# Performance work log

Measured on AMD Instinct MI355X. Metric: run time of the kernel, lower is better.

## Reference

```python
import jax, jax.numpy as jnp
import numpy as np

NPOINT = 2048
RADIUS = 0.4
NSAMPLE = 32
BN_EPS = 1e-5


def setup_inputs() -> dict:
    key = jax.random.key(0)
    ks = jax.random.split(key, 6)
    B, N, C = 8, 8192, 64
    xyz = jax.random.normal(ks[0], (B, N, 3), jnp.float32)
    points = jax.random.normal(ks[1], (B, N, C), jnp.float32)
    W1 = jax.random.normal(ks[2], (3 + C, 64), jnp.float32) * 0.1
    W2 = jax.random.normal(ks[3], (64, 64), jnp.float32) * 0.1
    W3 = jax.random.normal(ks[4], (64, 128), jnp.float32) * 0.1
    return dict(
        xyz=xyz, points=points,
        W1=W1, g1=jnp.ones(64), b1=jnp.zeros(64),
        W2=W2, g2=jnp.ones(64), b2=jnp.zeros(64),
        W3=W3, g3=jnp.ones(128), b3=jnp.zeros(128),
    )


def _furthest_point_sample(xyz, npoint):
    # xyz: (B, N, 3) -> (B, npoint) int32. Sequential max-min scan, batched.
    B, N, _ = xyz.shape

    def step(carry, _):
        dists, last = carry
        p = jnp.take_along_axis(xyz, last[:, None, None], axis=1)  # (B,1,3)
        d2 = jnp.sum((xyz - p) ** 2, axis=-1)                       # (B,N)
        dists = jnp.minimum(dists, d2)
        nxt = jnp.argmax(dists, axis=-1).astype(jnp.int32)
        return (dists, nxt), nxt

    init = (jnp.full((B, N), 1e10, xyz.dtype), jnp.zeros((B,), jnp.int32))
    _, idx = jax.lax.scan(step, init, None, length=npoint - 1)      # (npoint-1, B)
    idx = jnp.concatenate([jnp.zeros((1, B), jnp.int32), idx], axis=0)
    return idx.T                                                    # (B, npoint)


def _ball_query(xyz, new_xyz, radius, nsample):
    # For each centroid take the first nsample point indices (in original order)
    # within `radius`; pad with the first found index (CUDA ball_query semantics).
    B, N, _ = xyz.shape
    d2 = jnp.sum((new_xyz[:, :, None, :] - xyz[:, None, :, :]) ** 2, axis=-1)  # (B,S,N)
    mask = d2 < radius * radius
    key = jnp.where(mask, jnp.arange(N, dtype=jnp.int32), N)
    srt = jnp.sort(key, axis=-1)[..., :nsample]                     # (B,S,K)
    first = srt[..., :1]
    first = jnp.where(first == N, 0, first)                         # empty ball -> index 0
    return jnp.where(srt == N, first, srt)


def _gather(pts, idx):
    # pts: (B,N,D), idx: (B,...) -> (B,...,D)
    return jax.vmap(lambda p, i: p[i])(pts, idx)


def reference(xyz, points, W1, g1, b1, W2, g2, b2, W3, g3, b3):
    fps_idx = _furthest_point_sample(xyz, NPOINT)                   # (B,S)
    new_xyz = _gather(xyz, fps_idx)                                 # (B,S,3)
    idx = _ball_query(xyz, new_xyz, RADIUS, NSAMPLE)                # (B,S,K)
    grouped_xyz = _gather(xyz, idx) - new_xyz[:, :, None, :]        # (B,S,K,3)
    grouped_pts = _gather(points, idx)                              # (B,S,K,C)
    feats = jnp.concatenate([grouped_xyz, grouped_pts], axis=-1)    # (B,S,K,3+C)
    for W, g, b in ((W1, g1, b1), (W2, g2, b2), (W3, g3, b3)):
        feats = feats @ W                                           # 1x1 conv
        m = feats.mean(axis=(0, 1, 2))
        v = feats.var(axis=(0, 1, 2))                               # biased, torch BN train mode
        feats = g * (feats - m) * jax.lax.rsqrt(v + BN_EPS) + b
        feats = jax.nn.relu(feats)
    new_points = feats.max(axis=2)                                  # max over nsample -> (B,S,mlp[-1])
    return new_xyz, new_points
```

## Files before the change

kernel.cpp:

```cpp
#include <hip/hip_runtime.h>

constexpr int B_ = 8, N_ = 8192, NPOINT_ = 2048, NSAMPLE_ = 32;
constexpr int M_ROWS = B_ * NPOINT_ * NSAMPLE_;
constexpr int NGROUP = B_ * NPOINT_;
constexpr size_t OFF_NXF   = 0;
constexpr size_t OFF_IDX   = 196608;
constexpr size_t OFF_WF    = 1245184;
constexpr size_t OFF_GB    = 1311488;
constexpr size_t OFF_STATS = 1313536;
constexpr size_t OFF_NP    = 1315584;
constexpr size_t OFF_FLAG  = 1317632;
constexpr size_t OFF_MAXB  = 2097152;

__device__ __forceinline__ float bf2f(unsigned short u) {
  union { unsigned u; float f; } x; x.u = ((unsigned)u) << 16; return x.f;
}
__device__ __forceinline__ float lo16f(unsigned u) {
  union { unsigned u; float f; } x; x.u = u << 16; return x.f;
}
__device__ __forceinline__ float hi16f(unsigned u) {
  union { unsigned u; float f; } x; x.u = u & 0xffff0000u; return x.f;
}
__device__ __forceinline__ unsigned short f2bf(float f) {
  union { float f; unsigned u; } x; x.f = f;
  unsigned u = x.u + 0x7FFFu + ((x.u >> 16) & 1u);
  return (unsigned short)(u >> 16);
}
__device__ __forceinline__ void unpack8(uint4 u, float* x) {
  x[0] = bf2f((unsigned short)(u.x & 0xffffu)); x[1] = bf2f((unsigned short)(u.x >> 16));
  x[2] = bf2f((unsigned short)(u.y & 0xffffu)); x[3] = bf2f((unsigned short)(u.y >> 16));
  x[4] = bf2f((unsigned short)(u.z & 0xffffu)); x[5] = bf2f((unsigned short)(u.z >> 16));
  x[6] = bf2f((unsigned short)(u.w & 0xffffu)); x[7] = bf2f((unsigned short)(u.w >> 16));
}
__device__ __forceinline__ float ldf(const void* p, size_t i, bool bf) {
  return bf ? bf2f(((const unsigned short*)p)[i]) : ((const float*)p)[i];
}
__device__ __forceinline__ void stf(void* p, size_t i, bool bf, float v) {
  if (bf) ((unsigned short*)p)[i] = f2bf(v);
  else    ((float*)p)[i] = v;
}

extern "C" __global__ void detect_kernel(const unsigned short* __restrict__ xyz,
                                         int* __restrict__ flag) {
  if (threadIdx.x == 0 && blockIdx.x == 0) {
    int sane = 0;
    for (int k = 0; k < 32; ++k) {
      int e = (xyz[2 * k] >> 7) & 0xff;
      if (e >= 90 && e <= 140) ++sane;
    }
    *flag = (sane >= 24) ? 1 : 0;
  }
}

extern "C" __global__ void prep_kernel(
    const void* W1, const void* W2, const void* W3,
    const void* g1, const void* b1, const void* g2, const void* b2,
    const void* g3, const void* b3,
    float* __restrict__ wf, float* __restrict__ gb, const int* __restrict__ flag) {
  const bool bf = (*flag != 0);
  int i = blockIdx.x * 256 + threadIdx.x;
  if (i < 4288)       wf[i] = ldf(W1, i, bf);
  else if (i < 8384)  wf[i] = ldf(W2, i - 4288, bf);
  else if (i < 16576) wf[i] = ldf(W3, i - 8384, bf);
  else if (i < 17088) {
    int k = i - 16576; float v;
    if (k < 64)       v = ldf(g1, k, bf);
    else if (k < 128) v = ldf(b1, k - 64, bf);
    else if (k < 192) v = ldf(g2, k - 128, bf);
    else if (k < 256) v = ldf(b2, k - 192, bf);
    else if (k < 384) v = ldf(g3, k - 256, bf);
    else              v = ldf(b3, k - 384, bf);
    gb[k] = v;
  }
}

template <bool BF>
__device__ __forceinline__ void fps_body(
    const void* xyz, void* out, float* __restrict__ nxf,
    unsigned short* sxyz, float (*sv)[8], int (*si)[8]) {
#pragma clang fp contract(off)
  const int b = blockIdx.x;
  const int t = threadIdx.x;
  const int lane = t & 63, w = t >> 6;
  const size_t base = (size_t)b * N_ * 3;
  unsigned cc[24];
  float px[16], py[16], pz[16];
  float d[16];
  if (BF) {
    const uint4* xp = (const uint4*)((const unsigned short*)xyz + base) + t * 6;
    uint4* sp = (uint4*)sxyz + t * 6;
#pragma unroll
    for (int m = 0; m < 6; ++m) {
      uint4 u = xp[m];
      sp[m] = u;
      cc[4*m+0] = u.x; cc[4*m+1] = u.y; cc[4*m+2] = u.z; cc[4*m+3] = u.w;
    }
  } else {
#pragma unroll
    for (int k = 0; k < 16; ++k) {
      int i = t * 16 + k;
      px[k] = ((const float*)xyz)[base + i*3 + 0];
      py[k] = ((const float*)xyz)[base + i*3 + 1];
      pz[k] = ((const float*)xyz)[base + i*3 + 2];
    }
  }
#pragma unroll
  for (int k = 0; k < 16; ++k) d[k] = 1e10f;
  __syncthreads();
  float s0x=0.f,s0y=0.f,s0z=0.f, s1x=0.f,s1y=0.f,s1z=0.f,
        s2x=0.f,s2y=0.f,s2z=0.f, s3x=0.f,s3y=0.f,s3z=0.f;
  float p0, p1, p2;
  if (BF) { p0 = bf2f(sxyz[0]); p1 = bf2f(sxyz[1]); p2 = bf2f(sxyz[2]); }
  else {
    p0 = ((const float*)xyz)[base + 0];
    p1 = ((const float*)xyz)[base + 1];
    p2 = ((const float*)xyz)[base + 2];
  }
  if (t == 0) { s0x = p0; s0y = p1; s0z = p2; }
  for (int j = 1; j < NPOINT_; ++j) {
    if (BF) {
#pragma unroll
      for (int m = 0; m < 24; ++m) asm volatile("" : "+v"(cc[m]));
    } else {
#pragma unroll
      for (int k = 0; k < 16; ++k)
        asm volatile("" : "+v"(px[k]), "+v"(py[k]), "+v"(pz[k]));
    }
#pragma unroll
    for (int m = 0; m < 16; ++m) asm volatile("" : "+v"(d[m]));
    float bv = -1.0f;
#pragma unroll
    for (int k = 0; k < 16; ++k) {
      float x, y, z;
      if (BF) {
        if ((k & 1) == 0) {
          unsigned ra = cc[(3*k) >> 1], rb = cc[((3*k) >> 1) + 1];
          x = lo16f(ra); y = hi16f(ra); z = lo16f(rb);
        } else {
          unsigned ra = cc[(3*k - 1) >> 1], rb = cc[(3*k + 1) >> 1];
          x = hi16f(ra); y = lo16f(rb); z = hi16f(rb);
        }
      } else { x = px[k]; y = py[k]; z = pz[k]; }
      float dx = x - p0, dy = y - p1, dz = z - p2;
      float d2 = (dx*dx + dy*dy) + dz*dz;
      float dn = fminf(d[k], d2);
      d[k] = dn;
      bv = fmaxf(bv, dn);
    }
    float bv0 = bv;
#pragma unroll
    for (int off = 1; off < 64; off <<= 1)
      bv = fmaxf(bv, __shfl_xor(bv, off));
    int bk = 0;
    if (bv0 == bv) {
#pragma unroll
      for (int k = 15; k >= 0; --k)
        if (d[k] == bv0) bk = k;
    }
    unsigned long long m = __ballot(bv0 == bv);
    int sl = (int)__builtin_ctzll(m);
    int pi = __shfl(t * 16 + bk, sl);
    const int pb = j & 1;
    if (lane == 0) { sv[pb][w] = bv; si[pb][w] = pi; }
    __syncthreads();
    float gv = sv[pb][0]; int gpi = si[pb][0];
#pragma unroll
    for (int q = 1; q < 8; ++q) {
      float v2 = sv[pb][q]; int i2 = si[pb][q];
      if (v2 > gv) { gv = v2; gpi = i2; }
    }
    if (BF) {
      int wo3 = gpi * 3;
      p0 = bf2f(sxyz[wo3 + 0]); p1 = bf2f(sxyz[wo3 + 1]); p2 = bf2f(sxyz[wo3 + 2]);
    } else {
      size_t wo = base + (size_t)gpi * 3;
      p0 = ((const float*)xyz)[wo + 0];
      p1 = ((const float*)xyz)[wo + 1];
      p2 = ((const float*)xyz)[wo + 2];
    }
    if (t == (j & 511)) {
      const int s = j >> 9;
      if      (s == 0) { s0x = p0; s0y = p1; s0z = p2; }
      else if (s == 1) { s1x = p0; s1y = p1; s1z = p2; }
      else if (s == 2) { s2x = p0; s2y = p1; s2z = p2; }
      else             { s3x = p0; s3y = p1; s3z = p2; }
    }
  }
  const bool bfrt = BF;
#pragma unroll
  for (int s = 0; s < 4; ++s) {
    float cx = (s==0)?s0x:(s==1)?s1x:(s==2)?s2x:s3x;
    float cy = (s==0)?s0y:(s==1)?s1y:(s==2)?s2y:s3y;
    float cz = (s==0)?s0z:(s==1)?s1z:(s==2)?s2z:s3z;
    size_t o = ((size_t)b * NPOINT_ + s * 512 + t) * 3;
    nxf[o+0] = cx; nxf[o+1] = cy; nxf[o+2] = cz;
    stf(out, o+0, bfrt, cx); stf(out, o+1, bfrt, cy); stf(out, o+2, bfrt, cz);
  }
}

extern "C" __global__ void __launch_bounds__(512, 2) fps_kernel(
    const void* xyz, void* out, float* __restrict__ nxf,
    const int* __restrict__ flag) {
  __shared__ unsigned short sxyz[N_ * 3];
  __shared__ float sv[2][8];
  __shared__ int   si[2][8];
  if (*flag != 0) fps_body<true>(xyz, out, nxf, sxyz, sv, si);
  else            fps_body<false>(xyz, out, nxf, sxyz, sv, si);
}

extern "C" __global__ void __launch_bounds__(256) ballq_kernel(
    const void* xyz, const float* __restrict__ nxf,
    unsigned short* __restrict__ idxout, const int* __restrict__ flag) {
#pragma clang fp contract(off)
  const bool bf = (*flag != 0);
  const int gw = (int)((blockIdx.x * 256 + threadIdx.x) >> 6);
  const int lane = threadIdx.x & 63;
  const int b = gw >> 11;
  const int j = gw & (NPOINT_ - 1);
  const size_t base = (size_t)b * N_ * 3;
  const size_t co = ((size_t)b * NPOINT_ + j) * 3;
  const float c0 = nxf[co], c1 = nxf[co+1], c2 = nxf[co+2];
  unsigned short* out = idxout + (size_t)gw * NSAMPLE_;
  int cnt = 0, first = 0;
  for (int c = 0; c < N_/64 && cnt < NSAMPLE_; ++c) {
    int i = c * 64 + lane;
    float x = ldf(xyz, base + i*3 + 0, bf);
    float y = ldf(xyz, base + i*3 + 1, bf);
    float z = ldf(xyz, base + i*3 + 2, bf);
    float dx = x - c0, dy = y - c1, dz = z - c2;
    float d2 = (dx*dx + dy*dy) + dz*dz;
    unsigned long long m = __ballot(d2 < 0.16f);
    if (lane == 0) {
      while (m && cnt < NSAMPLE_) {
        int bit = __builtin_ctzll(m);
        int pi = c * 64 + bit;
        if (cnt == 0) first = pi;
        out[cnt] = (unsigned short)pi;
        ++cnt;
        m &= (m - 1);
      }
    }
    cnt = __shfl(cnt, 0);
  }
  first = __shfl(first, 0);
  if (lane >= cnt && lane < NSAMPLE_) out[lane] = (unsigned short)first;
}

__device__ __forceinline__ void l1_row(
    const void* xyz, const void* points, const float* __restrict__ nxf,
    const unsigned short* __restrict__ idx, const float* __restrict__ wf,
    int r, bool bf, float* acc) {
  const int b = r >> 16;
  const int j = (r >> 5) & (NPOINT_ - 1);
  const int i = idx[r];
  const size_t pt = (size_t)b * N_ + i;
  const float* cp = nxf + ((size_t)b * NPOINT_ + j) * 3;
  float f0 = ldf(xyz, pt*3 + 0, bf) - cp[0];
  float f1 = ldf(xyz, pt*3 + 1, bf) - cp[1];
  float f2 = ldf(xyz, pt*3 + 2, bf) - cp[2];
#pragma unroll
  for (int c = 0; c < 64; ++c)
    acc[c] = fmaf(f0, wf[c], fmaf(f1, wf[64+c], f2 * wf[128+c]));
  const float* wp = wf + 192;
  if (bf) {
    const uint4* pp = (const uint4*)((const unsigned short*)points + pt * 64);
#pragma unroll
    for (int s = 0; s < 8; ++s) {
      uint4 u = pp[s];
      float x[8]; unpack8(u, x);
#pragma unroll
      for (int kk = 0; kk < 8; ++kk)
#pragma unroll
        for (int c = 0; c < 64; ++c)
          acc[c] = fmaf(x[kk], wp[(s*8+kk)*64 + c], acc[c]);
    }
  } else {
    const float4* pp = (const float4*)((const float*)points + pt * 64);
#pragma unroll
    for (int s = 0; s < 16; ++s) {
      float4 u = pp[s];
      float x[4] = {u.x, u.y, u.z, u.w};
#pragma unroll
      for (int kk = 0; kk < 4; ++kk)
#pragma unroll
        for (int c = 0; c < 64; ++c)
          acc[c] = fmaf(x[kk], wp[(s*4+kk)*64 + c], acc[c]);
    }
  }
}

template <int LDW>
__device__ __forceinline__ void mm64(const float* v, const float* __restrict__ w,
                                     float* acc) {
#pragma unroll
  for (int ch = 0; ch < 64; ++ch)
#pragma unroll
    for (int c = 0; c < 64; ++c)
      acc[c] = fmaf(v[ch], w[ch*LDW + c], acc[c]);
}

__device__ __forceinline__ void bnrelu64(float* v, const float* __restrict__ np0) {
#pragma unroll
  for (int c = 0; c < 64; ++c)
    v[c] = fmaxf(fmaf(v[c], np0[c], np0[64 + c]), 0.f);
}

__device__ __forceinline__ void commit_stats64(float* a, float* __restrict__ stats) {
  float q[64];
#pragma unroll
  for (int c = 0; c < 64; ++c) q[c] = a[c] * a[c];
#pragma unroll
  for (int off = 1; off < 64; off <<= 1)
#pragma unroll
    for (int c = 0; c < 64; ++c) {
      a[c] += __shfl_xor(a[c], off);
      q[c] += __shfl_xor(q[c], off);
    }
  __shared__ float LS[4][64], LQ[4][64];
  const int t = threadIdx.x, w = t >> 6;
  if ((t & 63) == 0) {
#pragma unroll
    for (int c = 0; c < 64; ++c) { LS[w][c] = a[c]; LQ[w][c] = q[c]; }
  }
  __syncthreads();
  if (t < 64) {
    atomicAdd(&stats[t],      LS[0][t] + LS[1][t] + LS[2][t] + LS[3][t]);
    atomicAdd(&stats[64 + t], LQ[0][t] + LQ[1][t] + LQ[2][t] + LQ[3][t]);
  }
}

extern "C" __global__ void __launch_bounds__(256) p1_kernel(
    const void* xyz, const void* points, const float* __restrict__ nxf,
    const unsigned short* __restrict__ idx, const float* __restrict__ wf,
    float* __restrict__ stats, const int* __restrict__ flag) {
  const bool bf = (*flag != 0);
  const int r = blockIdx.x * 256 + threadIdx.x;
  float acc[64];
  l1_row(xyz, points, nxf, idx, wf, r, bf, acc);
  commit_stats64(acc, stats);
}

extern "C" __global__ void __launch_bounds__(256, 2) p2_kernel(
    const void* xyz, const void* points, const float* __restrict__ nxf,
    const unsigned short* __restrict__ idx, const float* __restrict__ wf,
    const float* __restrict__ w2, const float* __restrict__ np1,
    float* __restrict__ stats, const int* __restrict__ flag) {
  const bool bf = (*flag != 0);
  const int r = blockIdx.x * 256 + threadIdx.x;
  float v[64];
  l1_row(xyz, points, nxf, idx, wf, r, bf, v);
  bnrelu64(v, np1);
  float acc[64];
#pragma unroll
  for (int c = 0; c < 64; ++c) acc[c] = 0.f;
  mm64<64>(v, w2, acc);
  commit_stats64(acc, stats);
}

extern "C" __global__ void __launch_bounds__(256, 2) p3_kernel(
    const void* xyz, const void* points, const float* __restrict__ nxf,
    const unsigned short* __restrict__ idx, const float* __restrict__ wf,
    const float* __restrict__ w2, const float* __restrict__ w3,
    const float* __restrict__ np1, const float* __restrict__ np2,
    unsigned short* __restrict__ maxb, float* __restrict__ stats,
    const int* __restrict__ flag) {
  const bool bf = (*flag != 0);
  const int t = threadIdx.x, lane = t & 63, w = t >> 6;
  const int h = __builtin_amdgcn_readfirstlane(w & 1);
  const int g = blockIdx.x * 4 + (w >> 1) * 2 + (lane >> 5);
  const int r = g * 32 + (lane & 31);
  float v[64];
  l1_row(xyz, points, nxf, idx, wf, r, bf, v);
  bnrelu64(v, np1);
  float y2[64];
#pragma unroll
  for (int c = 0; c < 64; ++c) y2[c] = 0.f;
  mm64<64>(v, w2, y2);
  bnrelu64(y2, np2);
  const float* w3h = w3 + h * 64;
  float y3[64];
#pragma unroll
  for (int c = 0; c < 64; ++c) y3[c] = 0.f;
  mm64<128>(y2, w3h, y3);
  float* s = v; float* q = y2;
#pragma unroll
  for (int c = 0; c < 64; ++c) { s[c] = y3[c]; q[c] = y3[c] * y3[c]; }
#pragma unroll
  for (int off = 1; off <= 16; off <<= 1)
#pragma unroll
    for (int c = 0; c < 64; ++c)
      y3[c] = fmaxf(y3[c], __shfl_xor(y3[c], off));
  if ((lane & 31) == 0) {
    unsigned short* mo = maxb + (size_t)g * 128 + h * 64;
#pragma unroll
    for (int c = 0; c < 64; ++c) mo[c] = f2bf(y3[c]);
  }
#pragma unroll
  for (int off = 1; off < 64; off <<= 1)
#pragma unroll
    for (int c = 0; c < 64; ++c) {
      s[c] += __shfl_xor(s[c], off);
      q[c] += __shfl_xor(q[c], off);
    }
  __shared__ float LS[4][64], LQ[4][64];
  if (lane == 0) {
#pragma unroll
    for (int c = 0; c < 64; ++c) { LS[w][c] = s[c]; LQ[w][c] = q[c]; }
  }
  __syncthreads();
  if (t < 128) {
    int hh = t >> 6, cl = t & 63;
    atomicAdd(&stats[t],       LS[hh][cl] + LS[hh+2][cl]);
    atomicAdd(&stats[128 + t], LQ[hh][cl] + LQ[hh+2][cl]);
  }
}

extern "C" __global__ void nparam_kernel(
    const float* __restrict__ stats, const float* __restrict__ g,
    const float* __restrict__ bb, float* __restrict__ npar, int Cc) {
  int c = threadIdx.x;
  if (c < Cc) {
    float m = stats[c] * (1.0f / M_ROWS);
    float v = stats[Cc + c] * (1.0f / M_ROWS) - m * m;
    float sc = g[c] / sqrtf(v + 1e-5f);
    npar[c] = sc;
    npar[Cc + c] = bb[c] - m * sc;
  }
}

extern "C" __global__ void __launch_bounds__(256) final_kernel(
    const unsigned short* __restrict__ maxb, const float* __restrict__ npar,
    void* out, const int* __restrict__ flag) {
  const bool bf = (*flag != 0);
  const int gtid = blockIdx.x * 256 + threadIdx.x;
  const int c = gtid & 127;
  float y = bf2f(maxb[gtid]);
  float r = fmaxf(fmaf(y, npar[c], npar[128 + c]), 0.f);
  stf(out, (size_t)B_ * NPOINT_ * 3 + gtid, bf, r);
}

extern "C" void kernel_launch(void* const* d_in, const int* in_sizes, int n_in,
                              void* d_out, int out_size, void* d_ws, size_t ws_size,
                              hipStream_t stream) {
  const void* xyz    = d_in[0];
  const void* points = d_in[1];
  char* ws = (char*)d_ws;
  float* nxf   = (float*)(ws + OFF_NXF);
  unsigned short* wsIdx = (unsigned short*)(ws + OFF_IDX);
  float* wf    = (float*)(ws + OFF_WF);
  float* gb    = (float*)(ws + OFF_GB);
  float* stats = (float*)(ws + OFF_STATS);
  float* npar  = (float*)(ws + OFF_NP);
  int*   flag  = (int*)(ws + OFF_FLAG);
  unsigned short* maxb = (unsigned short*)(ws + OFF_MAXB);

  hipMemsetAsync(stats, 0, 512 * sizeof(float), stream);
  detect_kernel<<<1, 64, 0, stream>>>((const unsigned short*)xyz, flag);
  prep_kernel<<<67, 256, 0, stream>>>(d_in[2], d_in[5], d_in[8], d_in[3], d_in[4],
                                      d_in[6], d_in[7], d_in[9], d_in[10], wf, gb, flag);
  fps_kernel<<<B_, 512, 0, stream>>>(xyz, d_out, nxf, flag);
  ballq_kernel<<<(B_ * NPOINT_) / 4, 256, 0, stream>>>(xyz, nxf, wsIdx, flag);
  p1_kernel<<<M_ROWS / 256, 256, 0, stream>>>(xyz, points, nxf, wsIdx, wf, stats, flag);
  nparam_kernel<<<1, 128, 0, stream>>>(stats, gb, gb + 64, npar, 64);
  p2_kernel<<<M_ROWS / 256, 256, 0, stream>>>(xyz, points, nxf, wsIdx, wf, wf + 4288,
                                              npar, stats + 128, flag);
  nparam_kernel<<<1, 128, 0, stream>>>(stats + 128, gb + 128, gb + 192, npar + 128, 64);
  p3_kernel<<<(2 * M_ROWS) / 256, 256, 0, stream>>>(xyz, points, nxf, wsIdx, wf,
                                                    wf + 4288, wf + 8384, npar,
                                                    npar + 128, maxb, stats + 256, flag);
  nparam_kernel<<<1, 128, 0, stream>>>(stats + 256, gb + 256, gb + 384, npar + 256, 128);
  final_kernel<<<(NGROUP * 128) / 256, 256, 0, stream>>>(maxb, npar + 256, d_out, flag);
}
```

Before: 4.378 ms.

## Run FPS with 1024 threads per block and fuse argmax tracking into scan

The furthest-point-sampling kernel now uses 1024 threads per batch, so each thread holds 8 points instead of 16, and the cross-wave reduction covers 16 waves. The per-thread argmax index is tracked inside the distance loop rather than rescanned afterward, and the asm register-pinning barriers are removed. The aim is to shorten the per-iteration serial work on the critical FPS loop, which runs on only 8 blocks. In exchange the block-level reduction is longer, and the launch bounds change what register budget the compiler targets.

After: 4.235 ms. 1.03x faster.

```diff
diff --git a/kernel.cpp b/kernel.cpp
--- a/kernel.cpp
+++ b/kernel.cpp
@@ -77,38 +77,37 @@
 template <bool BF>
 __device__ __forceinline__ void fps_body(
     const void* xyz, void* out, float* __restrict__ nxf,
-    unsigned short* sxyz, float (*sv)[8], int (*si)[8]) {
+    unsigned short* sxyz, float (*sv)[16], int (*si)[16]) {
 #pragma clang fp contract(off)
   const int b = blockIdx.x;
   const int t = threadIdx.x;
   const int lane = t & 63, w = t >> 6;
   const size_t base = (size_t)b * N_ * 3;
-  unsigned cc[24];
-  float px[16], py[16], pz[16];
-  float d[16];
+  unsigned cc[12];
+  float px[8], py[8], pz[8];
+  float d[8];
   if (BF) {
-    const uint4* xp = (const uint4*)((const unsigned short*)xyz + base) + t * 6;
-    uint4* sp = (uint4*)sxyz + t * 6;
-#pragma unroll
-    for (int m = 0; m < 6; ++m) {
+    const uint4* xp = (const uint4*)((const unsigned short*)xyz + base) + t * 3;
+    uint4* sp = (uint4*)sxyz + t * 3;
+#pragma unroll
+    for (int m = 0; m < 3; ++m) {
       uint4 u = xp[m];
       sp[m] = u;
       cc[4*m+0] = u.x; cc[4*m+1] = u.y; cc[4*m+2] = u.z; cc[4*m+3] = u.w;
     }
   } else {
 #pragma unroll
-    for (int k = 0; k < 16; ++k) {
-      int i = t * 16 + k;
+    for (int k = 0; k < 8; ++k) {
+      int i = t * 8 + k;
       px[k] = ((const float*)xyz)[base + i*3 + 0];
       py[k] = ((const float*)xyz)[base + i*3 + 1];
       pz[k] = ((const float*)xyz)[base + i*3 + 2];
     }
   }
 #pragma unroll
-  for (int k = 0; k < 16; ++k) d[k] = 1e10f;
+  for (int k = 0; k < 8; ++k) d[k] = 1e10f;
   __syncthreads();
-  float s0x=0.f,s0y=0.f,s0z=0.f, s1x=0.f,s1y=0.f,s1z=0.f,
-        s2x=0.f,s2y=0.f,s2z=0.f, s3x=0.f,s3y=0.f,s3z=0.f;
+  float s0x=0.f,s0y=0.f,s0z=0.f, s1x=0.f,s1y=0.f,s1z=0.f;
   float p0, p1, p2;
   if (BF) { p0 = bf2f(sxyz[0]); p1 = bf2f(sxyz[1]); p2 = bf2f(sxyz[2]); }
   else {
@@ -118,19 +117,9 @@
   }
   if (t == 0) { s0x = p0; s0y = p1; s0z = p2; }
   for (int j = 1; j < NPOINT_; ++j) {
-    if (BF) {
-#pragma unroll
-      for (int m = 0; m < 24; ++m) asm volatile("" : "+v"(cc[m]));
-    } else {
-#pragma unroll
-      for (int k = 0; k < 16; ++k)
-        asm volatile("" : "+v"(px[k]), "+v"(py[k]), "+v"(pz[k]));
-    }
-#pragma unroll
-    for (int m = 0; m < 16; ++m) asm volatile("" : "+v"(d[m]));
-    float bv = -1.0f;
-#pragma unroll
-    for (int k = 0; k < 16; ++k) {
+    float bv = -1.0f; int bk = 0;
+#pragma unroll
+    for (int k = 0; k < 8; ++k) {
       float x, y, z;
       if (BF) {
         if ((k & 1) == 0) {
@@ -145,27 +134,21 @@
       float d2 = (dx*dx + dy*dy) + dz*dz;
       float dn = fminf(d[k], d2);
       d[k] = dn;
-      bv = fmaxf(bv, dn);
+      if (dn > bv) { bv = dn; bk = k; }
     }
     float bv0 = bv;
 #pragma unroll
     for (int off = 1; off < 64; off <<= 1)
       bv = fmaxf(bv, __shfl_xor(bv, off));
-    int bk = 0;
-    if (bv0 == bv) {
-#pragma unroll
-      for (int k = 15; k >= 0; --k)
-        if (d[k] == bv0) bk = k;
-    }
     unsigned long long m = __ballot(bv0 == bv);
     int sl = (int)__builtin_ctzll(m);
-    int pi = __shfl(t * 16 + bk, sl);
+    int pi = __shfl(t * 8 + bk, sl);
     const int pb = j & 1;
     if (lane == 0) { sv[pb][w] = bv; si[pb][w] = pi; }
     __syncthreads();
     float gv = sv[pb][0]; int gpi = si[pb][0];
 #pragma unroll
-    for (int q = 1; q < 8; ++q) {
+    for (int q = 1; q < 16; ++q) {
       float v2 = sv[pb][q]; int i2 = si[pb][q];
       if (v2 > gv) { gv = v2; gpi = i2; }
     }
@@ -178,32 +161,29 @@
       p1 = ((const float*)xyz)[wo + 1];
       p2 = ((const float*)xyz)[wo + 2];
     }
-    if (t == (j & 511)) {
-      const int s = j >> 9;
-      if      (s == 0) { s0x = p0; s0y = p1; s0z = p2; }
-      else if (s == 1) { s1x = p0; s1y = p1; s1z = p2; }
-      else if (s == 2) { s2x = p0; s2y = p1; s2z = p2; }
-      else             { s3x = p0; s3y = p1; s3z = p2; }
+    if (t == (j & 1023)) {
+      if ((j >> 10) == 0) { s0x = p0; s0y = p1; s0z = p2; }
+      else                { s1x = p0; s1y = p1; s1z = p2; }
     }
   }
   const bool bfrt = BF;
 #pragma unroll
-  for (int s = 0; s < 4; ++s) {
-    float cx = (s==0)?s0x:(s==1)?s1x:(s==2)?s2x:s3x;
-    float cy = (s==0)?s0y:(s==1)?s1y:(s==2)?s2y:s3y;
-    float cz = (s==0)?s0z:(s==1)?s1z:(s==2)?s2z:s3z;
-    size_t o = ((size_t)b * NPOINT_ + s * 512 + t) * 3;
+  for (int s = 0; s < 2; ++s) {
+    float cx = (s==0)?s0x:s1x;
+    float cy = (s==0)?s0y:s1y;
+    float cz = (s==0)?s0z:s1z;
+    size_t o = ((size_t)b * NPOINT_ + s * 1024 + t) * 3;
     nxf[o+0] = cx; nxf[o+1] = cy; nxf[o+2] = cz;
     stf(out, o+0, bfrt, cx); stf(out, o+1, bfrt, cy); stf(out, o+2, bfrt, cz);
   }
 }
 
-extern "C" __global__ void __launch_bounds__(512, 2) fps_kernel(
+extern "C" __global__ void __launch_bounds__(1024, 4) fps_kernel(
     const void* xyz, void* out, float* __restrict__ nxf,
     const int* __restrict__ flag) {
   __shared__ unsigned short sxyz[N_ * 3];
-  __shared__ float sv[2][8];
-  __shared__ int   si[2][8];
+  __shared__ float sv[2][16];
+  __shared__ int   si[2][16];
   if (*flag != 0) fps_body<true>(xyz, out, nxf, sxyz, sv, si);
   else            fps_body<false>(xyz, out, nxf, sxyz, sv, si);
 }
@@ -458,7 +438,7 @@
   detect_kernel<<<1, 64, 0, stream>>>((const unsigned short*)xyz, flag);
   prep_kernel<<<67, 256, 0, stream>>>(d_in[2], d_in[5], d_in[8], d_in[3], d_in[4],
                                       d_in[6], d_in[7], d_in[9], d_in[10], wf, gb, flag);
-  fps_kernel<<<B_, 512, 0, stream>>>(xyz, d_out, nxf, flag);
+  fps_kernel<<<B_, 1024, 0, stream>>>(xyz, d_out, nxf, flag);
   ballq_kernel<<<(B_ * NPOINT_) / 4, 256, 0, stream>>>(xyz, nxf, wsIdx, flag);
   p1_kernel<<<M_ROWS / 256, 256, 0, stream>>>(xyz, points, nxf, wsIdx, wf, stats, flag);
   nparam_kernel<<<1, 128, 0, stream>>>(stats, gb, gb + 64, npar, 64);
```
